# Kernel tuning notes

Hardware: AMD Instinct MI355X
Metric: run time of the kernel (lower is better)

The kernel has to match this reference:

```python
import jax, jax.numpy as jnp
import numpy as np

KE = 14.3996
ALPHA = 0.3
CUTOFF = 10.0
K_MAX = 6
N_ATOMS = 100000
N_PAIRS = 6400000
N_MOL = 64


def _generate_kvecs():
    kr = np.arange(0, K_MAX + 1, dtype=np.float32)
    kr = np.concatenate([kr, -kr[1:]])
    # cartesian product of (kr, kr, kr)
    g = np.stack(np.meshgrid(kr, kr, kr, indexing='ij'), axis=-1).reshape(-1, 3)
    norm = (g ** 2).sum(axis=1)
    mask = (norm <= K_MAX ** 2 + 2) & (norm != 0)
    return jnp.asarray(g[mask])  # [1020, 3]


def setup_inputs() -> dict:
    key = jax.random.key(0)
    k1, k2, k3, k4, k5, k6, k7 = jax.random.split(key, 7)
    partial_charges = jax.random.normal(k1, (N_ATOMS, 1), dtype=jnp.float32)
    # pair displacement vectors; scale so typical |r_ij| ~ 3-6 A, avoids d ~ 0
    Rij = jax.random.normal(k2, (N_PAIRS, 3), dtype=jnp.float32) * 3.0 + 1.0
    R = jax.random.uniform(k3, (N_ATOMS, 3), dtype=jnp.float32) * 20.0
    # orthorhombic-ish invertible cells: diag(~20) + small perturbation
    cell = jnp.eye(3, dtype=jnp.float32)[None] * 20.0 \
        + jax.random.uniform(k4, (N_MOL, 3, 3), dtype=jnp.float32) * 0.1
    idx_m = jnp.sort(jax.random.randint(k5, (N_ATOMS,), 0, N_MOL)).astype(jnp.int64)
    idx_i = jax.random.randint(k6, (N_PAIRS,), 0, N_ATOMS).astype(jnp.int64)
    idx_j = jax.random.randint(k7, (N_PAIRS,), 0, N_ATOMS).astype(jnp.int64)
    kvecs = _generate_kvecs()
    return {"partial_charges": partial_charges, "Rij": Rij, "R": R, "cell": cell,
            "kvecs": kvecs, "idx_m": idx_m, "idx_i": idx_i, "idx_j": idx_j}


def reference(partial_charges, Rij, R, cell, kvecs, idx_m, idx_i, idx_j):
    q = partial_charges.squeeze(-1)                      # [A]
    d_ij = jnp.linalg.norm(Rij, axis=1)                  # [P]
    sqrt_a = jnp.sqrt(jnp.float32(ALPHA))

    # ---- real space: gather q, erfc-screened pair potential, double scatter ----
    f_r = jax.scipy.special.erfc(sqrt_a * d_ij) / d_ij
    f_r_cut = jax.scipy.special.erfc(sqrt_a * CUTOFF) / CUTOFF
    pot_ij = q[idx_i] * q[idx_j] * (f_r - f_r_cut)
    pot_ij = jnp.where(d_ij <= CUTOFF, pot_ij, jnp.zeros_like(pot_ij))
    y_atom = jax.ops.segment_sum(pot_ij, idx_i, num_segments=N_ATOMS)
    y_real = 0.5 * KE * jax.ops.segment_sum(y_atom, idx_m, num_segments=N_MOL)

    # ---- reciprocal space ----
    two_pi = 2.0 * jnp.float32(np.pi)
    recip_box = two_pi * jnp.transpose(jnp.linalg.inv(cell), (0, 2, 1))  # [M,3,3]
    v_box = jnp.abs(jnp.linalg.det(cell))                                # [M]
    prefactor = two_pi / v_box
    kv = jnp.einsum('kd,mde->mke', kvecs, recip_box)     # [M,K,3]
    k_sq = jnp.sum(kv ** 2, axis=2)                      # [M,K]
    q_gauss = jnp.exp(-0.25 * k_sq / ALPHA)              # [M,K]
    # per-atom phase: gather per-molecule k-vectors, dot with positions
    kdp = jnp.einsum('akd,ad->ak', kv[idx_m], R)         # [A,K]
    q_real = jax.ops.segment_sum(q[:, None] * jnp.cos(kdp), idx_m, num_segments=N_MOL)
    q_imag = jax.ops.segment_sum(q[:, None] * jnp.sin(kdp), idx_m, num_segments=N_MOL)
    q_dens = q_real ** 2 + q_imag ** 2                   # [M,K]
    y_ewald = prefactor * jnp.sum(q_dens * q_gauss / k_sq, axis=1)
    self_int = jnp.sqrt(ALPHA / np.pi) * jax.ops.segment_sum(q ** 2, idx_m, num_segments=N_MOL)
    y_recip = KE * (y_ewald - self_int)

    return y_real + y_recip                              # [M]
```

## Files before the change

kernel.cpp:

```cpp
#include <hip/hip_runtime.h>
#include <math.h>

#define KE_C     14.3996f
#define ALPHA_C  0.3f
#define CUTOFF_C 10.0f
#define TWO_PI_C 6.283185307179586f
#define ASPL     32
#define NK2      512
#define NREAL    2048

typedef float vfloat4 __attribute__((ext_vector_type(4)));
typedef int   vint4   __attribute__((ext_vector_type(4)));

__device__ __forceinline__ float fast_erfc(float x) {
    float t = __builtin_amdgcn_rcpf(fmaf(0.3275911f, x, 1.0f));
    float p = fmaf(t, 1.061405429f, -1.453152027f);
    p = fmaf(t, p, 1.421413741f);
    p = fmaf(t, p, -0.284496736f);
    p = fmaf(t, p, 0.254829592f);
    return t * p * __expf(-x * x);
}

__device__ __forceinline__ void sincos_rev(float x, float* s, float* c) {
    float f = __builtin_amdgcn_fractf(x);
    *s = __builtin_amdgcn_sinf(f);
    *c = __builtin_amdgcn_cosf(f);
}

__device__ __forceinline__ float inv3x3(const float* c, float* inv) {
    float a00 = c[0], a01 = c[1], a02 = c[2];
    float a10 = c[3], a11 = c[4], a12 = c[5];
    float a20 = c[6], a21 = c[7], a22 = c[8];
    float det = a00 * (a11 * a22 - a12 * a21)
              - a01 * (a10 * a22 - a12 * a20)
              + a02 * (a10 * a21 - a11 * a20);
    float id = 1.0f / det;
    inv[0] = (a11 * a22 - a12 * a21) * id;
    inv[1] = (a02 * a21 - a01 * a22) * id;
    inv[2] = (a01 * a12 - a02 * a11) * id;
    inv[3] = (a12 * a20 - a10 * a22) * id;
    inv[4] = (a00 * a22 - a02 * a20) * id;
    inv[5] = (a02 * a10 - a00 * a12) * id;
    inv[6] = (a10 * a21 - a11 * a20) * id;
    inv[7] = (a01 * a20 - a00 * a21) * id;
    inv[8] = (a00 * a11 - a01 * a10) * id;
    return det;
}

__global__ __launch_bounds__(256) void k_setup(const float* __restrict__ R,
                                               const float* __restrict__ q,
                                               const int* __restrict__ idx_m,
                                               const float* __restrict__ cell,
                                               const float* __restrict__ kvecs,
                                               float4* __restrict__ S4,
                                               unsigned int* __restrict__ QP,
                                               float* __restrict__ SI,
                                               int* __restrict__ bounds,
                                               float4* __restrict__ KH,
                                               int* __restrict__ cnt,
                                               int natoms, int nmol, int nk, int NA) {
    int bid = blockIdx.x;
    int tid = threadIdx.x;
    if (bid < NA) {
        __shared__ float si[64];
        if (tid < 64) si[tid] = 0.0f;
        __syncthreads();
        int a = bid * 256 + tid;
        if (a < natoms) {
            int m = idx_m[a];
            float inv[9];
            inv3x3(cell + m * 9, inv);
            float r0 = R[3 * a], r1 = R[3 * a + 1], r2 = R[3 * a + 2];
            float s0 = inv[0] * r0 + inv[3] * r1 + inv[6] * r2;
            float s1 = inv[1] * r0 + inv[4] * r1 + inv[7] * r2;
            float s2 = inv[2] * r0 + inv[5] * r1 + inv[8] * r2;
            float qa = q[a];
            S4[a] = make_float4(s0, s1, s2, qa);
            QP[a] = (__float_as_uint(qa) & ~63u) | (unsigned int)(m & 63);
            atomicAdd(&si[m & 63], qa * qa);
        }
        __syncthreads();
        if (tid < 64) atomicAdd(&SI[tid], si[tid]);
    } else if (bid == NA) {
        int m = tid;
        if (m <= nmol) {
            int lo = 0, hi = natoms;
            while (lo < hi) {
                int mid = (lo + hi) >> 1;
                if (idx_m[mid] < m) lo = mid + 1; else hi = mid;
            }
            bounds[m] = lo;
        }
    } else {
        for (int k = tid; k < nk; k += 256) {
            float gx = kvecs[3 * k], gy = kvecs[3 * k + 1], gz = kvecs[3 * k + 2];
            bool pos = (gx > 0.5f) ||
                       (fabsf(gx) < 0.5f && (gy > 0.5f ||
                        (fabsf(gy) < 0.5f && gz > 0.5f)));
            if (pos) {
                int s = atomicAdd(cnt, 1);
                KH[s] = make_float4(gx, gy, gz, 0.0f);
            }
        }
    }
}

__global__ __launch_bounds__(256) void k_main(const float4* __restrict__ S4,
                                              const float4* __restrict__ KH,
                                              const int* __restrict__ bounds,
                                              float* __restrict__ QR,
                                              float* __restrict__ QI, int nrecip,
                                              const float* __restrict__ Rij,
                                              const int* __restrict__ idx_i,
                                              const int* __restrict__ idx_j,
                                              const unsigned int* __restrict__ QP,
                                              float* __restrict__ YRpad, int npairs) {
    __shared__ float acc[4][64];
    int tid = threadIdx.x;
    int bid = blockIdx.x;

    bool recip = (bid < 2 * nrecip) && (bid & 1);
    int idx = (bid < 2 * nrecip) ? (bid >> 1) : (bid - nrecip);

    if (recip) {
        int m  = idx / ASPL;
        int ac = idx % ASPL;
        int s0 = bounds[m], s1 = bounds[m + 1];
        int per = (s1 - s0 + ASPL - 1) / ASPL;
        int a0 = s0 + ac * per;
        int a1 = min(a0 + per, s1);
        float4 g0 = KH[tid];
        float4 g1 = KH[tid + 256];
        float qr0 = 0.f, qi0 = 0.f, qr1 = 0.f, qi1 = 0.f;
#pragma unroll 4
        for (int t = a0; t < a1; ++t) {
            float4 s = S4[t];
            float ph0 = fmaf(g0.x, s.x, fmaf(g0.y, s.y, g0.z * s.z));
            float ph1 = fmaf(g1.x, s.x, fmaf(g1.y, s.y, g1.z * s.z));
            float sn0, cs0, sn1, cs1;
            sincos_rev(ph0, &sn0, &cs0);
            sincos_rev(ph1, &sn1, &cs1);
            qr0 = fmaf(s.w, cs0, qr0);
            qi0 = fmaf(s.w, sn0, qi0);
            qr1 = fmaf(s.w, cs1, qr1);
            qi1 = fmaf(s.w, sn1, qi1);
        }
        atomicAdd(&QR[m * NK2 + tid], qr0);
        atomicAdd(&QI[m * NK2 + tid], qi0);
        atomicAdd(&QR[m * NK2 + tid + 256], qr1);
        atomicAdd(&QI[m * NK2 + tid + 256], qi1);
    } else {
        int wave = tid >> 6;
        ((float*)acc)[tid] = 0.0f;
        __syncthreads();
        const float sqa = 0.5477225575051661f;
        const float frcut = fast_erfc(sqa * CUTOFF_C) / CUTOFF_C;
        int nchunk = npairs >> 2;
        int stride = NREAL * 256;
        int c = idx * 256 + tid;
        vint4 ii, jj; vfloat4 A, B, C;
        if (c < nchunk) {
            int p = c << 2;
            ii = *(const vint4*)(idx_i + p);
            jj = *(const vint4*)(idx_j + p);
            const vfloat4* r4 = (const vfloat4*)(Rij + 3 * p);
            A = r4[0]; B = r4[1]; C = r4[2];
        }
        while (c < nchunk) {
            int cn = c + stride;
            vint4 ii2, jj2; vfloat4 A2, B2, C2;
            if (cn < nchunk) {
                int p = cn << 2;
                ii2 = *(const vint4*)(idx_i + p);
                jj2 = *(const vint4*)(idx_j + p);
                const vfloat4* r4 = (const vfloat4*)(Rij + 3 * p);
                A2 = r4[0]; B2 = r4[1]; C2 = r4[2];
            }
            unsigned int ui0 = QP[ii.x], ui1 = QP[ii.y], ui2 = QP[ii.z], ui3 = QP[ii.w];
            unsigned int uj0 = QP[jj.x], uj1 = QP[jj.y], uj2 = QP[jj.z], uj3 = QP[jj.w];
#define PAIR(xx, yy, zz, ui, uj)                                              \
            {                                                                 \
                float d2 = fmaf(xx, xx, fmaf(yy, yy, (zz) * (zz)));           \
                float rd = __builtin_amdgcn_rsqf(d2);                         \
                float d = d2 * rd;                                            \
                float f = fast_erfc(sqa * d) * rd - frcut;                    \
                f = (d2 <= CUTOFF_C * CUTOFF_C) ? f : 0.0f;                   \
                float qi_ = __uint_as_float((ui) & ~63u);                     \
                float qj_ = __uint_as_float((uj) & ~63u);                     \
                atomicAdd(&acc[wave][(ui) & 63u], qi_ * qj_ * f);             \
            }
            PAIR(A.x, A.y, A.z, ui0, uj0)
            PAIR(A.w, B.x, B.y, ui1, uj1)
            PAIR(B.z, B.w, C.x, ui2, uj2)
            PAIR(C.y, C.z, C.w, ui3, uj3)
#undef PAIR
            c = cn; ii = ii2; jj = jj2; A = A2; B = B2; C = C2;
        }
        if (bid == 0 && tid == 0) {
            for (int p = (npairs >> 2) << 2; p < npairs; ++p) {
                float x = Rij[3 * p], y = Rij[3 * p + 1], z = Rij[3 * p + 2];
                float d2 = fmaf(x, x, fmaf(y, y, z * z));
                if (d2 <= CUTOFF_C * CUTOFF_C) {
                    float rd = __builtin_amdgcn_rsqf(d2);
                    float d = d2 * rd;
                    unsigned int ui = QP[idx_i[p]], uj = QP[idx_j[p]];
                    float qi_ = __uint_as_float(ui & ~63u);
                    float qj_ = __uint_as_float(uj & ~63u);
                    atomicAdd(&acc[0][ui & 63u],
                              qi_ * qj_ * (fast_erfc(sqa * d) * rd - frcut));
                }
            }
        }
        __syncthreads();
        if (tid < 64) {
            float v = acc[0][tid] + acc[1][tid] + acc[2][tid] + acc[3][tid];
            atomicAdd(&YRpad[tid * 16], v);
        }
    }
}

__global__ __launch_bounds__(256) void k_final(const float4* __restrict__ KH,
                                               const int* __restrict__ cnt,
                                               const float* __restrict__ cell,
                                               const float* __restrict__ QR,
                                               const float* __restrict__ QI,
                                               const float* __restrict__ YRpad,
                                               const float* __restrict__ SI,
                                               float* __restrict__ out) {
    int m = blockIdx.x;
    int tid = threadIdx.x;
    __shared__ float wsum[4];
    float inv[9];
    float det = inv3x3(cell + m * 9, inv);
    int nhalf = cnt[0];
    float acc = 0.0f;
    for (int k = tid; k < nhalf; k += 256) {
        float4 g = KH[k];
        float kv0 = TWO_PI_C * (g.x * inv[0] + g.y * inv[1] + g.z * inv[2]);
        float kv1 = TWO_PI_C * (g.x * inv[3] + g.y * inv[4] + g.z * inv[5]);
        float kv2 = TWO_PI_C * (g.x * inv[6] + g.y * inv[7] + g.z * inv[8]);
        float ksq = kv0 * kv0 + kv1 * kv1 + kv2 * kv2;
        float qr = QR[m * NK2 + k], qi = QI[m * NK2 + k];
        acc += (qr * qr + qi * qi) * __expf(-0.25f / ALPHA_C * ksq) / ksq;
    }
#pragma unroll
    for (int off = 32; off > 0; off >>= 1) acc += __shfl_down(acc, off, 64);
    if ((tid & 63) == 0) wsum[tid >> 6] = acc;
    __syncthreads();
    if (tid == 0) {
        float s = 2.0f * (wsum[0] + wsum[1] + wsum[2] + wsum[3]);
        float pref = TWO_PI_C / fabsf(det);
        float self_c = sqrtf(ALPHA_C / 3.14159265358979323846f);
        out[m] = 0.5f * KE_C * YRpad[m * 16] + KE_C * (pref * s - self_c * SI[m]);
    }
}

extern "C" void kernel_launch(void* const* d_in, const int* in_sizes, int n_in,
                              void* d_out, int out_size, void* d_ws, size_t ws_size,
                              hipStream_t stream) {
    const float* q     = (const float*)d_in[0];
    const float* Rij   = (const float*)d_in[1];
    const float* R     = (const float*)d_in[2];
    const float* cell  = (const float*)d_in[3];
    const float* kvecs = (const float*)d_in[4];
    const int*   idx_m = (const int*)d_in[5];
    const int*   idx_i = (const int*)d_in[6];
    const int*   idx_j = (const int*)d_in[7];

    int natoms = in_sizes[0];
    int npairs = in_sizes[1] / 3;
    int nmol   = in_sizes[3] / 9;
    int nk     = in_sizes[4] / 3;
    float* out = (float*)d_out;

    float*  W      = (float*)d_ws;
    int*    bounds = (int*)W;
    float4* S4     = (float4*)(W + 80);
    unsigned int* QP = (unsigned int*)(W + 80 + 4 * (size_t)natoms);
    size_t  zoff   = 80 + 5 * (size_t)natoms;
    zoff = (zoff + 3) & ~(size_t)3;
    float4* KH     = (float4*)(W + zoff);
    float*  QR     = W + zoff + 4 * NK2;
    float*  QI     = QR + (size_t)nmol * NK2;
    float*  SI     = QI + (size_t)nmol * NK2;
    float*  YRpad  = SI + 64;
    int*    cnt    = (int*)(YRpad + 64 * 16);
    size_t zero_bytes = (4 * NK2 + (size_t)2 * nmol * NK2 + 64 + 64 * 16 + 4) * sizeof(float);
    (void)hipMemsetAsync(KH, 0, zero_bytes, stream);

    int NA = (natoms + 255) / 256;
    int nrecip = nmol * ASPL;
    k_setup<<<NA + 2, 256, 0, stream>>>(R, q, idx_m, cell, kvecs, S4, QP, SI,
                                        bounds, KH, cnt, natoms, nmol, nk, NA);
    k_main <<<nrecip + NREAL, 256, 0, stream>>>(S4, KH, bounds, QR, QI, nrecip,
                                                Rij, idx_i, idx_j, QP, YRpad, npairs);
    k_final<<<nmol, 256, 0, stream>>>(KH, cnt, cell, QR, QI, YRpad, SI, out);
}
```

Measured before the change: 270.2 us.

## Split fused recip/real kernel into separate launches and use exact erfc

Splits the combined reciprocal/real-space kernel into two separate launches, so the two workloads no longer share one grid. The real-space kernel drops the manual software prefetch, the fast erfc polynomial and rsq tricks in favour of library erfcf, sqrtf and division, uses branches instead of selects, and sets a minimum occupancy in its launch bounds. Per-atom charge and molecule are stored as a float2 instead of a bit-packed uint. This loses overlap between the compute-bound recip work and the memory-bound real work, widens the gathered data, and uses costlier math in the pair loop.

```diff
diff --git a/kernel.cpp b/kernel.cpp
--- a/kernel.cpp
+++ b/kernel.cpp
@@ -11,15 +11,6 @@
 
 typedef float vfloat4 __attribute__((ext_vector_type(4)));
 typedef int   vint4   __attribute__((ext_vector_type(4)));
-
-__device__ __forceinline__ float fast_erfc(float x) {
-    float t = __builtin_amdgcn_rcpf(fmaf(0.3275911f, x, 1.0f));
-    float p = fmaf(t, 1.061405429f, -1.453152027f);
-    p = fmaf(t, p, 1.421413741f);
-    p = fmaf(t, p, -0.284496736f);
-    p = fmaf(t, p, 0.254829592f);
-    return t * p * __expf(-x * x);
-}
 
 __device__ __forceinline__ void sincos_rev(float x, float* s, float* c) {
     float f = __builtin_amdgcn_fractf(x);
@@ -53,7 +44,7 @@
                                                const float* __restrict__ cell,
                                                const float* __restrict__ kvecs,
                                                float4* __restrict__ S4,
-                                               unsigned int* __restrict__ QP,
+                                               float2* __restrict__ QM,
                                                float* __restrict__ SI,
                                                int* __restrict__ bounds,
                                                float4* __restrict__ KH,
@@ -76,7 +67,7 @@
             float s2 = inv[2] * r0 + inv[5] * r1 + inv[8] * r2;
             float qa = q[a];
             S4[a] = make_float4(s0, s1, s2, qa);
-            QP[a] = (__float_as_uint(qa) & ~63u) | (unsigned int)(m & 63);
+            QM[a] = make_float2(qa, __int_as_float(m));
             atomicAdd(&si[m & 63], qa * qa);
         }
         __syncthreads();
@@ -105,117 +96,100 @@
     }
 }
 
-__global__ __launch_bounds__(256) void k_main(const float4* __restrict__ S4,
-                                              const float4* __restrict__ KH,
-                                              const int* __restrict__ bounds,
-                                              float* __restrict__ QR,
-                                              float* __restrict__ QI, int nrecip,
-                                              const float* __restrict__ Rij,
-                                              const int* __restrict__ idx_i,
-                                              const int* __restrict__ idx_j,
-                                              const unsigned int* __restrict__ QP,
-                                              float* __restrict__ YRpad, int npairs) {
+__global__ __launch_bounds__(256) void k_recip(const float4* __restrict__ S4,
+                                               const float4* __restrict__ KH,
+                                               const int* __restrict__ bounds,
+                                               float* __restrict__ QR,
+                                               float* __restrict__ QI) {
+    int tid = threadIdx.x;
+    int bid = blockIdx.x;
+    int m  = bid / ASPL;
+    int ac = bid % ASPL;
+    int s0 = bounds[m], s1 = bounds[m + 1];
+    int per = (s1 - s0 + ASPL - 1) / ASPL;
+    int a0 = s0 + ac * per;
+    int a1 = min(a0 + per, s1);
+    float4 g0 = KH[tid];
+    float4 g1 = KH[tid + 256];
+    float qr0 = 0.f, qi0 = 0.f, qr1 = 0.f, qi1 = 0.f;
+#pragma unroll 4
+    for (int t = a0; t < a1; ++t) {
+        float4 s = S4[t];
+        float ph0 = fmaf(g0.x, s.x, fmaf(g0.y, s.y, g0.z * s.z));
+        float ph1 = fmaf(g1.x, s.x, fmaf(g1.y, s.y, g1.z * s.z));
+        float sn0, cs0, sn1, cs1;
+        sincos_rev(ph0, &sn0, &cs0);
+        sincos_rev(ph1, &sn1, &cs1);
+        qr0 = fmaf(s.w, cs0, qr0);
+        qi0 = fmaf(s.w, sn0, qi0);
+        qr1 = fmaf(s.w, cs1, qr1);
+        qi1 = fmaf(s.w, sn1, qi1);
+    }
+    atomicAdd(&QR[m * NK2 + tid], qr0);
+    atomicAdd(&QI[m * NK2 + tid], qi0);
+    atomicAdd(&QR[m * NK2 + tid + 256], qr1);
+    atomicAdd(&QI[m * NK2 + tid + 256], qi1);
+}
+
+__global__ __launch_bounds__(256, 8) void k_real(const float* __restrict__ Rij,
+                                                 const int* __restrict__ idx_i,
+                                                 const int* __restrict__ idx_j,
+                                                 const float2* __restrict__ QM,
+                                                 float* __restrict__ YRpad, int npairs) {
     __shared__ float acc[4][64];
     int tid = threadIdx.x;
-    int bid = blockIdx.x;
-
-    bool recip = (bid < 2 * nrecip) && (bid & 1);
-    int idx = (bid < 2 * nrecip) ? (bid >> 1) : (bid - nrecip);
-
-    if (recip) {
-        int m  = idx / ASPL;
-        int ac = idx % ASPL;
-        int s0 = bounds[m], s1 = bounds[m + 1];
-        int per = (s1 - s0 + ASPL - 1) / ASPL;
-        int a0 = s0 + ac * per;
-        int a1 = min(a0 + per, s1);
-        float4 g0 = KH[tid];
-        float4 g1 = KH[tid + 256];
-        float qr0 = 0.f, qi0 = 0.f, qr1 = 0.f, qi1 = 0.f;
-#pragma unroll 4
-        for (int t = a0; t < a1; ++t) {
-            float4 s = S4[t];
-            float ph0 = fmaf(g0.x, s.x, fmaf(g0.y, s.y, g0.z * s.z));
-            float ph1 = fmaf(g1.x, s.x, fmaf(g1.y, s.y, g1.z * s.z));
-            float sn0, cs0, sn1, cs1;
-            sincos_rev(ph0, &sn0, &cs0);
-            sincos_rev(ph1, &sn1, &cs1);
-            qr0 = fmaf(s.w, cs0, qr0);
-            qi0 = fmaf(s.w, sn0, qi0);
-            qr1 = fmaf(s.w, cs1, qr1);
-            qi1 = fmaf(s.w, sn1, qi1);
-        }
-        atomicAdd(&QR[m * NK2 + tid], qr0);
-        atomicAdd(&QI[m * NK2 + tid], qi0);
-        atomicAdd(&QR[m * NK2 + tid + 256], qr1);
-        atomicAdd(&QI[m * NK2 + tid + 256], qi1);
-    } else {
-        int wave = tid >> 6;
-        ((float*)acc)[tid] = 0.0f;
-        __syncthreads();
-        const float sqa = 0.5477225575051661f;
-        const float frcut = fast_erfc(sqa * CUTOFF_C) / CUTOFF_C;
-        int nchunk = npairs >> 2;
-        int stride = NREAL * 256;
-        int c = idx * 256 + tid;
-        vint4 ii, jj; vfloat4 A, B, C;
-        if (c < nchunk) {
-            int p = c << 2;
-            ii = *(const vint4*)(idx_i + p);
-            jj = *(const vint4*)(idx_j + p);
-            const vfloat4* r4 = (const vfloat4*)(Rij + 3 * p);
-            A = r4[0]; B = r4[1]; C = r4[2];
-        }
-        while (c < nchunk) {
-            int cn = c + stride;
-            vint4 ii2, jj2; vfloat4 A2, B2, C2;
-            if (cn < nchunk) {
-                int p = cn << 2;
-                ii2 = *(const vint4*)(idx_i + p);
-                jj2 = *(const vint4*)(idx_j + p);
-                const vfloat4* r4 = (const vfloat4*)(Rij + 3 * p);
-                A2 = r4[0]; B2 = r4[1]; C2 = r4[2];
+    int wave = tid >> 6;
+    acc[wave][tid & 63] = 0.0f;
+    __syncthreads();
+    const float sqa = 0.5477225575051661f;
+    const float frcut = erfcf(sqa * CUTOFF_C) / CUTOFF_C;
+    int nchunk = npairs >> 2;
+    int stride = NREAL * 256;
+    for (int c = blockIdx.x * 256 + tid; c < nchunk; c += stride) {
+        int p = c << 2;
+        vint4 ii = *(const vint4*)(idx_i + p);
+        vint4 jj = *(const vint4*)(idx_j + p);
+        const vfloat4* r4 = (const vfloat4*)(Rij + 3 * p);
+        vfloat4 ra = r4[0], rb = r4[1], rc = r4[2];
+        float x0 = ra.x, y0 = ra.y, z0 = ra.z;
+        float x1 = ra.w, y1 = rb.x, z1 = rb.y;
+        float x2 = rb.z, y2 = rb.w, z2 = rc.x;
+        float x3 = rc.y, y3 = rc.z, z3 = rc.w;
+        float2 qi0 = QM[ii.x], qi1 = QM[ii.y], qi2 = QM[ii.z], qi3 = QM[ii.w];
+        float2 qj0 = QM[jj.x], qj1 = QM[jj.y], qj2 = QM[jj.z], qj3 = QM[jj.w];
+        float d0 = sqrtf(x0 * x0 + y0 * y0 + z0 * z0);
+        float d1 = sqrtf(x1 * x1 + y1 * y1 + z1 * z1);
+        float d2 = sqrtf(x2 * x2 + y2 * y2 + z2 * z2);
+        float d3 = sqrtf(x3 * x3 + y3 * y3 + z3 * z3);
+        if (d0 <= CUTOFF_C)
+            atomicAdd(&acc[wave][__float_as_int(qi0.y) & 63],
+                      qi0.x * qj0.x * (erfcf(sqa * d0) / d0 - frcut));
+        if (d1 <= CUTOFF_C)
+            atomicAdd(&acc[wave][__float_as_int(qi1.y) & 63],
+                      qi1.x * qj1.x * (erfcf(sqa * d1) / d1 - frcut));
+        if (d2 <= CUTOFF_C)
+            atomicAdd(&acc[wave][__float_as_int(qi2.y) & 63],
+                      qi2.x * qj2.x * (erfcf(sqa * d2) / d2 - frcut));
+        if (d3 <= CUTOFF_C)
+            atomicAdd(&acc[wave][__float_as_int(qi3.y) & 63],
+                      qi3.x * qj3.x * (erfcf(sqa * d3) / d3 - frcut));
+    }
+    if (blockIdx.x == 0 && tid == 0) {
+        for (int p = (npairs >> 2) << 2; p < npairs; ++p) {
+            float x = Rij[3 * p], y = Rij[3 * p + 1], z = Rij[3 * p + 2];
+            float d = sqrtf(x * x + y * y + z * z);
+            if (d <= CUTOFF_C) {
+                float2 qi = QM[idx_i[p]];
+                float2 qj = QM[idx_j[p]];
+                atomicAdd(&acc[0][__float_as_int(qi.y) & 63],
+                          qi.x * qj.x * (erfcf(sqa * d) / d - frcut));
             }
-            unsigned int ui0 = QP[ii.x], ui1 = QP[ii.y], ui2 = QP[ii.z], ui3 = QP[ii.w];
-            unsigned int uj0 = QP[jj.x], uj1 = QP[jj.y], uj2 = QP[jj.z], uj3 = QP[jj.w];
-#define PAIR(xx, yy, zz, ui, uj)                                              \
-            {                                                                 \
-                float d2 = fmaf(xx, xx, fmaf(yy, yy, (zz) * (zz)));           \
-                float rd = __builtin_amdgcn_rsqf(d2);                         \
-                float d = d2 * rd;                                            \
-                float f = fast_erfc(sqa * d) * rd - frcut;                    \
-                f = (d2 <= CUTOFF_C * CUTOFF_C) ? f : 0.0f;                   \
-                float qi_ = __uint_as_float((ui) & ~63u);                     \
-                float qj_ = __uint_as_float((uj) & ~63u);                     \
-                atomicAdd(&acc[wave][(ui) & 63u], qi_ * qj_ * f);             \
-            }
-            PAIR(A.x, A.y, A.z, ui0, uj0)
-            PAIR(A.w, B.x, B.y, ui1, uj1)
-            PAIR(B.z, B.w, C.x, ui2, uj2)
-            PAIR(C.y, C.z, C.w, ui3, uj3)
-#undef PAIR
-            c = cn; ii = ii2; jj = jj2; A = A2; B = B2; C = C2;
-        }
-        if (bid == 0 && tid == 0) {
-            for (int p = (npairs >> 2) << 2; p < npairs; ++p) {
-                float x = Rij[3 * p], y = Rij[3 * p + 1], z = Rij[3 * p + 2];
-                float d2 = fmaf(x, x, fmaf(y, y, z * z));
-                if (d2 <= CUTOFF_C * CUTOFF_C) {
-                    float rd = __builtin_amdgcn_rsqf(d2);
-                    float d = d2 * rd;
-                    unsigned int ui = QP[idx_i[p]], uj = QP[idx_j[p]];
-                    float qi_ = __uint_as_float(ui & ~63u);
-                    float qj_ = __uint_as_float(uj & ~63u);
-                    atomicAdd(&acc[0][ui & 63u],
-                              qi_ * qj_ * (fast_erfc(sqa * d) * rd - frcut));
-                }
-            }
-        }
-        __syncthreads();
-        if (tid < 64) {
-            float v = acc[0][tid] + acc[1][tid] + acc[2][tid] + acc[3][tid];
-            atomicAdd(&YRpad[tid * 16], v);
-        }
+        }
+    }
+    __syncthreads();
+    if (tid < 64) {
+        float v = acc[0][tid] + acc[1][tid] + acc[2][tid] + acc[3][tid];
+        atomicAdd(&YRpad[tid * 16], v);
     }
 }
 
@@ -276,8 +250,8 @@
     float*  W      = (float*)d_ws;
     int*    bounds = (int*)W;
     float4* S4     = (float4*)(W + 80);
-    unsigned int* QP = (unsigned int*)(W + 80 + 4 * (size_t)natoms);
-    size_t  zoff   = 80 + 5 * (size_t)natoms;
+    float2* QM     = (float2*)(W + 80 + 4 * (size_t)natoms);
+    size_t  zoff   = 80 + 6 * (size_t)natoms;
     zoff = (zoff + 3) & ~(size_t)3;
     float4* KH     = (float4*)(W + zoff);
     float*  QR     = W + zoff + 4 * NK2;
@@ -289,10 +263,9 @@
     (void)hipMemsetAsync(KH, 0, zero_bytes, stream);
 
     int NA = (natoms + 255) / 256;
-    int nrecip = nmol * ASPL;
-    k_setup<<<NA + 2, 256, 0, stream>>>(R, q, idx_m, cell, kvecs, S4, QP, SI,
+    k_setup<<<NA + 2, 256, 0, stream>>>(R, q, idx_m, cell, kvecs, S4, QM, SI,
                                         bounds, KH, cnt, natoms, nmol, nk, NA);
-    k_main <<<nrecip + NREAL, 256, 0, stream>>>(S4, KH, bounds, QR, QI, nrecip,
-                                                Rij, idx_i, idx_j, QP, YRpad, npairs);
+    k_recip<<<nmol * ASPL, 256, 0, stream>>>(S4, KH, bounds, QR, QI);
+    k_real <<<NREAL, 256, 0, stream>>>(Rij, idx_i, idx_j, QM, YRpad, npairs);
     k_final<<<nmol, 256, 0, stream>>>(KH, cnt, cell, QR, QI, YRpad, SI, out);
 }
```

New measurement: 240.6 us. -11.0%, faster.
